# Kernel optimization log

Hardware: AMD Instinct MI355X
Metric: run time of the kernel (lower is better)

## Reference

```python
import jax, jax.numpy as jnp
from jax import lax
import numpy as np

N_NODES = 5000
N_EDGES = 80000
N_FEAT = 128
N_TPLT = 16
TPLT_NODES = 10
N_FW = 3         # Frank-Wolfe (conditional-gradient) outer iterations
SINK_ITERS = 10  # log-domain Sinkhorn inner iterations


def setup_inputs() -> dict:
    key = jax.random.key(0)
    k1, k2, k3, k4, k5 = jax.random.split(key, 5)
    x = jax.random.normal(k1, (N_NODES, N_FEAT), jnp.float32)
    src = jax.random.randint(k2, (N_EDGES,), 0, N_NODES, jnp.int32)
    dst = jax.random.randint(k3, (N_EDGES,), 0, N_NODES, jnp.int32)
    edge_index = jnp.stack([src, dst], axis=0)
    A0 = jax.random.uniform(k4, (N_TPLT, TPLT_NODES, TPLT_NODES), jnp.float32)
    tplt_adjacencies = 0.5 * (A0 + jnp.transpose(A0, (0, 2, 1)))  # symmetrized, as in template_initialisation
    tplt_features = jax.random.normal(k5, (N_TPLT, TPLT_NODES, N_FEAT), jnp.float32)
    q0 = jnp.zeros((N_TPLT, TPLT_NODES), jnp.float32)   # softmax(q0) -> uniform template node weights
    alpha0 = jnp.zeros((1,), jnp.float32)               # sigmoid(alpha0) -> alpha = 0.5
    return {"x": x, "edge_index": edge_index, "tplt_adjacencies": tplt_adjacencies,
            "tplt_features": tplt_features, "q0": q0, "alpha0": alpha0}


def _sinkhorn_log(G, logp, logq, reg):
    """Log-domain Sinkhorn solving min <G,T> + reg*KL(T | p q^T); returns T [N, m]."""
    def step(carry, _):
        f, g = carry
        f = reg * (logp - jax.scipy.special.logsumexp((g[None, :] - G) / reg, axis=1))
        g = reg * (logq - jax.scipy.special.logsumexp((f[:, None] - G) / reg, axis=0))
        return (f, g), None
    (f, g), _ = lax.scan(step, (jnp.zeros_like(logp), jnp.zeros_like(logq)), None, length=SINK_ITERS)
    return jnp.exp((f[:, None] + g[None, :] - G) / reg)


def _fgw_dist(A, x, p, C2, F2, q, alpha):
    """Fused Gromov-Wasserstein distance (square loss) between graph (A, x, p)
    and one template (C2, F2, q), solved by conditional gradient with Sinkhorn
    inner OT solves and exact quadratic line search."""
    # pairwise squared-euclidean feature cost M [N, m]
    M = jnp.sum(x * x, 1)[:, None] + jnp.sum(F2 * F2, 1)[None, :] - 2.0 * (x @ F2.T)
    # square-loss Gromov decomposition: L(C1,C2) (x) T = constC - 2 * C1 T C2
    constC = ((A * A) @ p)[:, None] + ((C2 * C2) @ q)[None, :]
    logp, logq = jnp.log(p), jnp.log(q)
    T0 = p[:, None] * q[None, :]

    def fw_step(T, _):
        ATC = A @ (T @ C2)                        # [N, m]
        tens = constC - 2.0 * ATC
        G = (1.0 - alpha) * M + 2.0 * alpha * tens  # linearized gradient
        reg = 0.05 * jnp.mean(jnp.abs(G)) + 1e-9
        Tn = _sinkhorn_log(G, logp, logq, reg)
        dT = Tn - T
        AdTC = A @ (dT @ C2)
        # cost(T + g*dT) = a g^2 + b g + c  (square-loss FGW)
        a = -2.0 * alpha * jnp.sum(AdTC * dT)
        b = (1.0 - alpha) * jnp.sum(M * dT) + alpha * (jnp.sum(constC * dT) - 4.0 * jnp.sum(ATC * dT))
        gamma = jnp.where(a > 0.0, jnp.clip(-b / (2.0 * a + 1e-16), 0.0, 1.0),
                          jnp.where(a + b < 0.0, 1.0, 0.0))
        return T + gamma * dT, None

    T, _ = lax.scan(fw_step, T0, None, length=N_FW)
    ATC = A @ (T @ C2)
    return (1.0 - alpha) * jnp.sum(M * T) + alpha * (jnp.sum(constC * T) - 2.0 * jnp.sum(ATC * T))


def reference(x, edge_index, tplt_adjacencies, tplt_features, q0, alpha0):
    N = x.shape[0]
    # dense adjacency from COO edge list (to_dense_adj equivalent)
    A = jnp.zeros((N, N), x.dtype).at[edge_index[0], edge_index[1]].set(1.0)
    p = jnp.full((N,), 1.0 / N, x.dtype)       # uniform graph node weights
    alpha = jax.nn.sigmoid(alpha0[0])          # trained FGW trade-off (multi_alpha=False)
    q = jax.nn.softmax(q0, axis=1)             # trained template node weights
    dists = jax.vmap(lambda C2, F2, qk: _fgw_dist(A, x, p, C2, F2, qk, alpha))(
        tplt_adjacencies, tplt_features, q)
    return dists  # [n_tplt] FGW-distance embedding of the graph
```

## Files before the change

### kernel.cpp

```cpp
#include <hip/hip_runtime.h>
#include <stdint.h>

typedef float    f32x4 __attribute__((ext_vector_type(4)));
typedef uint32_t u32x4 __attribute__((ext_vector_type(4)));

#define NN 5000
#define NE 80000
#define NF 128
#define NT 16
#define TN 10
#define NFW 3
#define NSK 10
#define PW (1.0f/5000.0f)
#define RB 128
#define GRX 40
#define TPB 1024
#define NSL 5

#define OFF_DEG  0u
#define OFF_RP   20224u
#define OFF_CUR  40448u
#define OFF_COL  60672u
#define OFF_SCG  380672u
#define OFF_M    384000u
#define OFF_T    4224000u
#define OFF_ATM  8064000u
#define OFF_ATT  9344000u
#define OFF_DTM  9664000u
#define OFF_DTT  10944000u
#define OFF_Y2M  11264000u
#define OFF_Y2T  12544000u
#define OFF_ADM  12864000u
#define OFF_ADT  14144000u

#define L_YM   0
#define L_YT   80000
#define L_RED  100000
#define L_WLS  101024
#define L_UNI  101088
#define SMEM_BYTES 101280

__device__ __forceinline__ uint32_t bfb(float x) {
  uint32_t u = __float_as_uint(x);
  return (u + 0x7fffu + ((u >> 16) & 1u)) >> 16;
}
__device__ __forceinline__ uint32_t pk(float a, float b) { return bfb(a) | (bfb(b) << 16); }
__device__ __forceinline__ float ubl(uint32_t u) { return __uint_as_float(u << 16); }
__device__ __forceinline__ float ubh(uint32_t u) { return __uint_as_float(u & 0xffff0000u); }
__device__ __forceinline__ float sigm(float z) { return 1.f / (1.f + __expf(-z)); }

__device__ __forceinline__ void ld12(const float* p, float* v) {
  f32x4 a = *(const f32x4*)p, b = *(const f32x4*)(p + 4), c = *(const f32x4*)(p + 8);
  v[0]=a[0]; v[1]=a[1]; v[2]=a[2]; v[3]=a[3]; v[4]=b[0]; v[5]=b[1]; v[6]=b[2]; v[7]=b[3];
  v[8]=c[0]; v[9]=c[1];
}
__device__ __forceinline__ void st12(float* p, const float* v) {
  *(f32x4*)p       = (f32x4){v[0], v[1], v[2], v[3]};
  *(f32x4*)(p + 4) = (f32x4){v[4], v[5], v[6], v[7]};
  *(f32x4*)(p + 8) = (f32x4){v[8], v[9], 0.f, 0.f};
}
__device__ __forceinline__ void ldbf(const u32x4* __restrict__ M4, const uint32_t* __restrict__ M1,
                                     size_t i, float* v) {
  u32x4 A = M4[i]; uint32_t B = M1[i];
  v[0]=ubl(A[0]); v[1]=ubh(A[0]); v[2]=ubl(A[1]); v[3]=ubh(A[1]);
  v[4]=ubl(A[2]); v[5]=ubh(A[2]); v[6]=ubl(A[3]); v[7]=ubh(A[3]);
  v[8]=ubl(B);    v[9]=ubh(B);
}
__device__ __forceinline__ void stbf(u32x4* __restrict__ M4, uint32_t* __restrict__ M1,
                                     size_t i, const float* v) {
  M4[i] = (u32x4){pk(v[0], v[1]), pk(v[2], v[3]), pk(v[4], v[5]), pk(v[6], v[7])};
  M1[i] = pk(v[8], v[9]);
}
__device__ __forceinline__ float bred16(float v, float* red) {
  #pragma unroll
  for (int o = 32; o; o >>= 1) v += __shfl_xor(v, o, 64);
  __syncthreads();
  if ((threadIdx.x & 63) == 0) red[threadIdx.x >> 6] = v;
  __syncthreads();
  float r = 0.f;
  #pragma unroll
  for (int w = 0; w < 16; ++w) r += red[w];
  return r;
}

__global__ void k_init(int* __restrict__ deg) {
  int i = blockIdx.x * 256 + threadIdx.x;
  if (i < NN) deg[i] = 0;
}
__global__ void k_deg(const int* __restrict__ ei, int* __restrict__ deg) {
  int e = blockIdx.x * 256 + threadIdx.x;
  if (e < NE) atomicAdd(&deg[ei[e]], 1);
}
__global__ void k_scan(const int* __restrict__ deg, int* __restrict__ rowptr, int* __restrict__ cur) {
  __shared__ int scr[1024];
  int tid = threadIdx.x;
  int loc[5], s = 0;
  #pragma unroll
  for (int r = 0; r < 5; ++r) {
    int idx = tid * 5 + r;
    int d = (idx < NN) ? deg[idx] : 0;
    loc[r] = s; s += d;
  }
  scr[tid] = s; __syncthreads();
  for (int off = 1; off < 1024; off <<= 1) {
    int v = scr[tid];
    int u = (tid >= off) ? scr[tid - off] : 0;
    __syncthreads();
    scr[tid] = v + u;
    __syncthreads();
  }
  int base = (tid > 0) ? scr[tid - 1] : 0;
  #pragma unroll
  for (int r = 0; r < 5; ++r) {
    int idx = tid * 5 + r;
    if (idx < NN) { int v = base + loc[r]; rowptr[idx] = v; cur[idx] = v; }
  }
  if (tid == 1023) rowptr[NN] = scr[1023];
}
__global__ void k_fill(const int* __restrict__ ei, int* __restrict__ cur, int* __restrict__ col) {
  int e = blockIdx.x * 256 + threadIdx.x;
  if (e < NE) {
    int s = ei[e];
    int pos = atomicAdd(&cur[s], 1);
    col[pos] = ei[NE + e];
  }
}
__global__ void kM(const float* __restrict__ x, const float* __restrict__ F2,
                   float* __restrict__ Mb) {
  __shared__ float ffs[TN];
  const int k = blockIdx.y, tid = threadIdx.x;
  const int i = blockIdx.x * RB + tid;
  const float* Fk = F2 + (size_t)k * TN * NF;
  if (tid < TN) {
    float s = 0.f;
    for (int d = 0; d < NF; ++d) { float f = Fk[tid * NF + d]; s += f * f; }
    ffs[tid] = s;
  }
  __syncthreads();
  if (i >= NN) return;
  const f32x4* xr = (const f32x4*)(x + (size_t)i * NF);
  float acc[TN];
  #pragma unroll
  for (int j = 0; j < TN; ++j) acc[j] = 0.f;
  float xsq = 0.f;
  for (int dc = 0; dc < NF / 4; ++dc) {
    f32x4 xv = xr[dc];
    xsq += xv[0]*xv[0] + xv[1]*xv[1] + xv[2]*xv[2] + xv[3]*xv[3];
    #pragma unroll
    for (int j = 0; j < TN; ++j) {
      const float* Fj = Fk + j * NF + dc * 4;
      acc[j] += xv[0]*Fj[0] + xv[1]*Fj[1] + xv[2]*Fj[2] + xv[3]*Fj[3];
    }
  }
  float v[TN];
  #pragma unroll
  for (int j = 0; j < TN; ++j) v[j] = xsq + ffs[j] - 2.f * acc[j];
  st12(Mb + ((size_t)k * NN + i) * 12, v);
}

__device__ __forceinline__ void uni_setup(const float* __restrict__ q0,
                                          const float* __restrict__ C2k, int k,
                                          float* qvs, float* c2qs, float* qC2s) {
  const int tid = threadIdx.x;
  if (tid < TN) {
    float mx = -1e30f, e[TN], s = 0.f;
    #pragma unroll
    for (int j = 0; j < TN; ++j) mx = fmaxf(mx, q0[k * TN + j]);
    #pragma unroll
    for (int j = 0; j < TN; ++j) { e[j] = __expf(q0[k * TN + j] - mx); s += e[j]; }
    float inv = 1.f / s;
    qvs[tid] = e[tid] * inv;
    float c2 = 0.f, qc = 0.f;
    #pragma unroll
    for (int l = 0; l < TN; ++l) {
      float c = C2k[tid * TN + l];
      c2 += c * c * e[l] * inv;
      qc += e[l] * inv * C2k[l * TN + tid];
    }
    c2qs[tid] = c2; qC2s[tid] = qc;
  }
  __syncthreads();
}

__global__ __launch_bounds__(TPB) void kFW(
    const int* __restrict__ rowptr, const int* __restrict__ col,
    const float* __restrict__ Mb, float* __restrict__ Tb,
    u32x4* __restrict__ AtM, uint32_t* __restrict__ AtT,
    u32x4* __restrict__ DtM, uint32_t* __restrict__ DtT,
    u32x4* __restrict__ Y2M, uint32_t* __restrict__ Y2T,
    u32x4* __restrict__ AdM, uint32_t* __restrict__ AdT_,
    const float* __restrict__ q0, const float* __restrict__ C2g,
    const float* __restrict__ a0p, float* __restrict__ scg, int t) {
  extern __shared__ char smem[];
  u32x4* LYM = (u32x4*)(smem + L_YM);
  uint32_t* LYT = (uint32_t*)(smem + L_YT);
  float* red = (float*)(smem + L_RED);
  float* wls = (float*)(smem + L_WLS);
  float* qvs = (float*)(smem + L_UNI);
  float* c2qs = qvs + 16; float* qC2s = qvs + 32;

  const int k = blockIdx.x, tid = threadIdx.x;
  const float* C2k = C2g + k * 100;
  uni_setup(q0, C2k, k, qvs, c2qs, qC2s);
  const float alpha = sigm(a0p[0]), oma = 1.f - alpha;
  const size_t kb = (size_t)k * NN;

  float gamma = 0.f;
  if (t > 0) {
    for (int i = tid; i < NN; i += TPB) { LYM[i] = Y2M[kb + i]; LYT[i] = Y2T[kb + i]; }
    __syncthreads();
    float bA = 0.f, aA = 0.f;
    for (int s = 0; s < NSL; ++s) {
      int r = s * TPB + tid;
      if (r < NN) {
        int e0 = rowptr[r], e1 = rowptr[r + 1];
        float adt[TN];
        #pragma unroll
        for (int j = 0; j < TN; ++j) adt[j] = 0.f;
        for (int e = e0; e < e1; ++e) {
          int c = col[e];
          u32x4 A = LYM[c]; uint32_t B = LYT[c];
          adt[0] += ubl(A[0]); adt[1] += ubh(A[0]); adt[2] += ubl(A[1]); adt[3] += ubh(A[1]);
          adt[4] += ubl(A[2]); adt[5] += ubh(A[2]); adt[6] += ubl(A[3]); adt[7] += ubh(A[3]);
          adt[8] += ubl(B);    adt[9] += ubh(B);
        }
        float av[TN], dv[TN];
        ldbf(AtM, AtT, kb + r, av); ldbf(DtM, DtT, kb + r, dv);
        #pragma unroll
        for (int j = 0; j < TN; ++j) { bA += av[j] * dv[j]; aA += adt[j] * dv[j]; }
        stbf(AdM, AdT_, kb + r, adt);
      }
    }
    bA = bred16(bA, red); aA = bred16(aA, red);
    const float bM = scg[k * 2 + 0], bC = scg[k * 2 + 1];
    float a_ = -2.f * alpha * aA;
    float b_ = oma * bM + alpha * (bC - 4.f * bA);
    gamma = (a_ > 0.f) ? fminf(fmaxf(-b_ / (2.f * a_ + 1e-16f), 0.f), 1.f)
                       : ((a_ + b_ < 0.f) ? 1.f : 0.f);
    for (int s = 0; s < NSL; ++s) {
      int r = s * TPB + tid;
      if (r < NN) {
        float tv[TN], dv[TN], av[TN], adt[TN];
        ld12(Tb + (kb + r) * 12, tv);
        ldbf(DtM, DtT, kb + r, dv);
        ldbf(AtM, AtT, kb + r, av);
        ldbf(AdM, AdT_, kb + r, adt);
        #pragma unroll
        for (int j = 0; j < TN; ++j) { tv[j] += gamma * dv[j]; av[j] += gamma * adt[j]; }
        st12(Tb + (kb + r) * 12, tv);
        stbf(AtM, AtT, kb + r, av);
      }
    }
  } else {
    for (int s = 0; s < NSL; ++s) {
      int r = s * TPB + tid;
      if (r < NN) {
        float dg = (float)(rowptr[r + 1] - rowptr[r]) * PW;
        float tv[TN], av[TN];
        #pragma unroll
        for (int j = 0; j < TN; ++j) { tv[j] = PW * qvs[j]; av[j] = dg * qC2s[j]; }
        st12(Tb + (kb + r) * 12, tv);
        stbf(AtM, AtT, kb + r, av);
      }
    }
  }

  float sabs = 0.f;
  for (int s = 0; s < NSL; ++s) {
    int r = s * TPB + tid;
    if (r < NN) {
      float mv[TN], av[TN];
      ld12(Mb + (kb + r) * 12, mv); ldbf(AtM, AtT, kb + r, av);
      float cc = (float)(rowptr[r + 1] - rowptr[r]) * PW;
      #pragma unroll
      for (int j = 0; j < TN; ++j)
        sabs += fabsf(oma * mv[j] + 2.f * alpha * (cc + c2qs[j] - 2.f * av[j]));
    }
  }
  sabs = bred16(sabs, red);
  const float invreg = 1.f / (0.05f * sabs * (1.f / (float)(NN * TN)) + 1e-9f);

  for (int s = 0; s < NSL; ++s) {
    int r = s * TPB + tid;
    if (r < NN) {
      float mv[TN], av[TN], G[TN];
      ld12(Mb + (kb + r) * 12, mv); ldbf(AtM, AtT, kb + r, av);
      float cc = (float)(rowptr[r + 1] - rowptr[r]) * PW;
      #pragma unroll
      for (int j = 0; j < TN; ++j)
        G[j] = oma * mv[j] + 2.f * alpha * (cc + c2qs[j] - 2.f * av[j]);
      float mn = G[0];
      #pragma unroll
      for (int j = 1; j < TN; ++j) mn = fminf(mn, G[j]);
      #pragma unroll
      for (int j = 0; j < TN; ++j) G[j] = __expf(-(G[j] - mn) * invreg);
      stbf(LYM, LYT, (size_t)r, G);
    }
  }
  __syncthreads();

  float wl[TN], wp[TN];
  #pragma unroll
  for (int j = 0; j < TN; ++j) { wl[j] = 1.f; wp[j] = 1.f; }
  for (int it = 0; it < NSK; ++it) {
    float csl[TN];
    #pragma unroll
    for (int j = 0; j < TN; ++j) csl[j] = 0.f;
    for (int s = 0; s < NSL; ++s) {
      int r = s * TPB + tid;
      if (r < NN) {
        float E[TN];
        ldbf(LYM, LYT, (size_t)r, E);
        float dot = 0.f;
        #pragma unroll
        for (int j = 0; j < TN; ++j) dot += E[j] * wl[j];
        float u = PW * __builtin_amdgcn_rcpf(fmaxf(dot, 1e-35f));
        #pragma unroll
        for (int j = 0; j < TN; ++j) csl[j] += E[j] * u;
      }
    }
    #pragma unroll
    for (int j = 0; j < TN; ++j) {
      float vv = csl[j];
      #pragma unroll
      for (int o = 32; o; o >>= 1) vv += __shfl_xor(vv, o, 64);
      if ((tid & 63) == j) red[(tid >> 6) * 16 + j] = vv;
    }
    __syncthreads();
    if (tid < TN) {
      float ssum = 0.f;
      #pragma unroll
      for (int w = 0; w < 16; ++w) ssum += red[w * 16 + tid];
      wls[tid] = qvs[tid] * __builtin_amdgcn_rcpf(fmaxf(ssum, 1e-35f));
    }
    __syncthreads();
    #pragma unroll
    for (int j = 0; j < TN; ++j) { wp[j] = wl[j]; wl[j] = wls[j]; }
  }

  float bM = 0.f, bC = 0.f;
  for (int s = 0; s < NSL; ++s) {
    int r = s * TPB + tid;
    if (r < NN) {
      float E[TN];
      ldbf(LYM, LYT, (size_t)r, E);
      float dot = 0.f;
      #pragma unroll
      for (int j = 0; j < TN; ++j) dot += E[j] * wp[j];
      float u = PW * __builtin_amdgcn_rcpf(fmaxf(dot, 1e-35f));
      float tv[TN], mv[TN], dT[TN];
      ld12(Tb + (kb + r) * 12, tv);
      ld12(Mb + (kb + r) * 12, mv);
      float cc = (float)(rowptr[r + 1] - rowptr[r]) * PW;
      #pragma unroll
      for (int j = 0; j < TN; ++j) {
        float tn = u * E[j] * wl[j];
        dT[j] = tn - tv[j];
        bM += mv[j] * dT[j];
        bC += (cc + c2qs[j]) * dT[j];
      }
      stbf(DtM, DtT, kb + r, dT);
      float y[TN];
      #pragma unroll
      for (int j = 0; j < TN; ++j) {
        float ss = 0.f;
        #pragma unroll
        for (int l = 0; l < TN; ++l) ss += dT[l] * C2k[l * TN + j];
        y[j] = ss;
      }
      stbf(Y2M, Y2T, kb + r, y);
    }
  }
  bM = bred16(bM, red); bC = bred16(bC, red);
  if (tid == 0) { scg[k * 2 + 0] = bM; scg[k * 2 + 1] = bC; }
}

__global__ __launch_bounds__(TPB) void kFin(
    const int* __restrict__ rowptr, const int* __restrict__ col,
    const float* __restrict__ Mb, const float* __restrict__ Tb,
    const u32x4* __restrict__ AtM, const uint32_t* __restrict__ AtT,
    const u32x4* __restrict__ DtM, const uint32_t* __restrict__ DtT,
    const u32x4* __restrict__ Y2M, const uint32_t* __restrict__ Y2T,
    u32x4* __restrict__ AdM, uint32_t* __restrict__ AdT_,
    const float* __restrict__ q0, const float* __restrict__ C2g,
    const float* __restrict__ a0p, const float* __restrict__ scg,
    float* __restrict__ out) {
  extern __shared__ char smem[];
  u32x4* LYM = (u32x4*)(smem + L_YM);
  uint32_t* LYT = (uint32_t*)(smem + L_YT);
  float* red = (float*)(smem + L_RED);
  float* qvs = (float*)(smem + L_UNI);
  float* c2qs = qvs + 16; float* qC2s = qvs + 32;

  const int k = blockIdx.x, tid = threadIdx.x;
  const float* C2k = C2g + k * 100;
  uni_setup(q0, C2k, k, qvs, c2qs, qC2s);
  const float alpha = sigm(a0p[0]), oma = 1.f - alpha;
  const size_t kb = (size_t)k * NN;

  for (int i = tid; i < NN; i += TPB) { LYM[i] = Y2M[kb + i]; LYT[i] = Y2T[kb + i]; }
  __syncthreads();
  float bA = 0.f, aA = 0.f;
  for (int s = 0; s < NSL; ++s) {
    int r = s * TPB + tid;
    if (r < NN) {
      int e0 = rowptr[r], e1 = rowptr[r + 1];
      float adt[TN];
      #pragma unroll
      for (int j = 0; j < TN; ++j) adt[j] = 0.f;
      for (int e = e0; e < e1; ++e) {
        int c = col[e];
        u32x4 A = LYM[c]; uint32_t B = LYT[c];
        adt[0] += ubl(A[0]); adt[1] += ubh(A[0]); adt[2] += ubl(A[1]); adt[3] += ubh(A[1]);
        adt[4] += ubl(A[2]); adt[5] += ubh(A[2]); adt[6] += ubl(A[3]); adt[7] += ubh(A[3]);
        adt[8] += ubl(B);    adt[9] += ubh(B);
      }
      float av[TN], dv[TN];
      ldbf(AtM, AtT, kb + r, av); ldbf(DtM, DtT, kb + r, dv);
      #pragma unroll
      for (int j = 0; j < TN; ++j) { bA += av[j] * dv[j]; aA += adt[j] * dv[j]; }
      stbf(AdM, AdT_, kb + r, adt);
    }
  }
  bA = bred16(bA, red); aA = bred16(aA, red);
  const float bM = scg[k * 2 + 0], bC = scg[k * 2 + 1];
  float a_ = -2.f * alpha * aA;
  float b_ = oma * bM + alpha * (bC - 4.f * bA);
  float gamma = (a_ > 0.f) ? fminf(fmaxf(-b_ / (2.f * a_ + 1e-16f), 0.f), 1.f)
                           : ((a_ + b_ < 0.f) ? 1.f : 0.f);
  float d1 = 0.f, d2 = 0.f, d3 = 0.f;
  for (int s = 0; s < NSL; ++s) {
    int r = s * TPB + tid;
    if (r < NN) {
      float tv[TN], dv[TN], av[TN], adt[TN], mv[TN];
      ld12(Tb + (kb + r) * 12, tv);
      ldbf(DtM, DtT, kb + r, dv);
      ldbf(AtM, AtT, kb + r, av);
      ldbf(AdM, AdT_, kb + r, adt);
      ld12(Mb + (kb + r) * 12, mv);
      float cc = (float)(rowptr[r + 1] - rowptr[r]) * PW;
      #pragma unroll
      for (int j = 0; j < TN; ++j) {
        float Tf = tv[j] + gamma * dv[j];
        float Af = av[j] + gamma * adt[j];
        d1 += mv[j] * Tf;
        d2 += (cc + c2qs[j]) * Tf;
        d3 += Af * Tf;
      }
    }
  }
  d1 = bred16(d1, red); d2 = bred16(d2, red); d3 = bred16(d3, red);
  if (tid == 0) out[k] = oma * d1 + alpha * (d2 - 2.f * d3);
}

extern "C" void kernel_launch(void* const* d_in, const int* in_sizes, int n_in,
                              void* d_out, int out_size, void* d_ws, size_t ws_size,
                              hipStream_t stream) {
  const float* x  = (const float*)d_in[0];
  const int*   ei = (const int*)d_in[1];
  const float* C2 = (const float*)d_in[2];
  const float* F2 = (const float*)d_in[3];
  const float* q0 = (const float*)d_in[4];
  const float* a0p = (const float*)d_in[5];
  float* out = (float*)d_out;

  char* ws = (char*)d_ws;
  int* deg    = (int*)(ws + OFF_DEG);
  int* rowptr = (int*)(ws + OFF_RP);
  int* cur    = (int*)(ws + OFF_CUR);
  int* col    = (int*)(ws + OFF_COL);
  float* scg  = (float*)(ws + OFF_SCG);
  float* Mb   = (float*)(ws + OFF_M);
  float* Tb   = (float*)(ws + OFF_T);
  u32x4* AtM  = (u32x4*)(ws + OFF_ATM);
  uint32_t* AtT = (uint32_t*)(ws + OFF_ATT);
  u32x4* DtM  = (u32x4*)(ws + OFF_DTM);
  uint32_t* DtT = (uint32_t*)(ws + OFF_DTT);
  u32x4* Y2M  = (u32x4*)(ws + OFF_Y2M);
  uint32_t* Y2T = (uint32_t*)(ws + OFF_Y2T);
  u32x4* AdM  = (u32x4*)(ws + OFF_ADM);
  uint32_t* AdT_ = (uint32_t*)(ws + OFF_ADT);

  hipFuncSetAttribute((const void*)kFW, hipFuncAttributeMaxDynamicSharedMemorySize, SMEM_BYTES);
  hipFuncSetAttribute((const void*)kFin, hipFuncAttributeMaxDynamicSharedMemorySize, SMEM_BYTES);

  k_init<<<(NN + 255) / 256, 256, 0, stream>>>(deg);
  k_deg<<<(NE + 255) / 256, 256, 0, stream>>>(ei, deg);
  k_scan<<<1, 1024, 0, stream>>>(deg, rowptr, cur);
  k_fill<<<(NE + 255) / 256, 256, 0, stream>>>(ei, cur, col);
  kM<<<dim3(GRX, NT), RB, 0, stream>>>(x, F2, Mb);

  for (int t = 0; t < NFW; ++t)
    kFW<<<NT, TPB, SMEM_BYTES, stream>>>(rowptr, col, Mb, Tb, AtM, AtT, DtM, DtT,
                                         Y2M, Y2T, AdM, AdT_, q0, C2, a0p, scg, t);
  kFin<<<NT, TPB, SMEM_BYTES, stream>>>(rowptr, col, Mb, Tb, AtM, AtT, DtM, DtT,
                                        Y2M, Y2T, AdM, AdT_, q0, C2, a0p, scg, out);
}
```

Baseline: 439.0 us.

## Split per-template FW kernel into multi-block stages with atomic cross-block reductions

Replaces the single 16-block kernel, which ran one 1024-thread block per template, with separate stage kernels. The gather A·ΔT (kA), the gradient/T update (kB) and the final objective (kFin) each run on a 40x16 grid, and the Sinkhorn kernel kD uses 16 blocks per template that each write only their own slice of rows. Partial sums are combined through global atomics, and a last-block counter produces the final output. M and the gradient are stored in fp16 to cut memory traffic. This spreads the work across far more CUs, at the cost of extra launches, redundant Sinkhorn iterations in every block of a template, and lower precision for M and G.

```diff
diff --git a/kernel.cpp b/kernel.cpp
--- a/kernel.cpp
+++ b/kernel.cpp
@@ -1,4 +1,5 @@
 #include <hip/hip_runtime.h>
+#include <hip/hip_fp16.h>
 #include <stdint.h>
 
 typedef float    f32x4 __attribute__((ext_vector_type(4)));
@@ -14,31 +15,37 @@
 #define PW (1.0f/5000.0f)
 #define RB 128
 #define GRX 40
-#define TPB 1024
-#define NSL 5
+#define DTPB 512
+#define DSL 10
+#define NBD 16
+#define RPD 313
 
 #define OFF_DEG  0u
 #define OFF_RP   20224u
 #define OFF_CUR  40448u
 #define OFF_COL  60672u
-#define OFF_SCG  380672u
-#define OFF_M    384000u
-#define OFF_T    4224000u
-#define OFF_ATM  8064000u
-#define OFF_ATT  9344000u
-#define OFF_DTM  9664000u
-#define OFF_DTT  10944000u
-#define OFF_Y2M  11264000u
-#define OFF_Y2T  12544000u
-#define OFF_ADM  12864000u
-#define OFF_ADT  14144000u
-
-#define L_YM   0
-#define L_YT   80000
+#define OFF_SC   380672u
+#define SC_FLOATS 384
+#define OFF_MM   382272u
+#define OFF_MT   1662272u
+#define OFF_T    1982272u
+#define OFF_ATM  5822272u
+#define OFF_ATT  7102272u
+#define OFF_DTM  7422272u
+#define OFF_DTT  8702272u
+#define OFF_Y2M  9022272u
+#define OFF_Y2T  10302272u
+#define OFF_ADM  10622272u
+#define OFF_ADT  11902272u
+#define OFF_GM   12222272u
+#define OFF_GT   13502272u
+
+#define L_EM   0
+#define L_ET   80000
 #define L_RED  100000
-#define L_WLS  101024
-#define L_UNI  101088
-#define SMEM_BYTES 101280
+#define L_WLS  100512
+#define L_UNI  100576
+#define SMEM_D 100768
 
 __device__ __forceinline__ uint32_t bfb(float x) {
   uint32_t u = __float_as_uint(x);
@@ -47,6 +54,16 @@
 __device__ __forceinline__ uint32_t pk(float a, float b) { return bfb(a) | (bfb(b) << 16); }
 __device__ __forceinline__ float ubl(uint32_t u) { return __uint_as_float(u << 16); }
 __device__ __forceinline__ float ubh(uint32_t u) { return __uint_as_float(u & 0xffff0000u); }
+__device__ __forceinline__ uint32_t pkh(float a, float b) {
+  return (uint32_t)__half_as_ushort(__float2half(a)) |
+         ((uint32_t)__half_as_ushort(__float2half(b)) << 16);
+}
+__device__ __forceinline__ float ulh(uint32_t u) {
+  return __half2float(__ushort_as_half((unsigned short)(u & 0xffffu)));
+}
+__device__ __forceinline__ float uhh(uint32_t u) {
+  return __half2float(__ushort_as_half((unsigned short)(u >> 16)));
+}
 __device__ __forceinline__ float sigm(float z) { return 1.f / (1.f + __expf(-z)); }
 
 __device__ __forceinline__ void ld12(const float* p, float* v) {
@@ -71,7 +88,20 @@
   M4[i] = (u32x4){pk(v[0], v[1]), pk(v[2], v[3]), pk(v[4], v[5]), pk(v[6], v[7])};
   M1[i] = pk(v[8], v[9]);
 }
-__device__ __forceinline__ float bred16(float v, float* red) {
+__device__ __forceinline__ void ldhf(const u32x4* __restrict__ M4, const uint32_t* __restrict__ M1,
+                                     size_t i, float* v) {
+  u32x4 A = M4[i]; uint32_t B = M1[i];
+  v[0]=ulh(A[0]); v[1]=uhh(A[0]); v[2]=ulh(A[1]); v[3]=uhh(A[1]);
+  v[4]=ulh(A[2]); v[5]=uhh(A[2]); v[6]=ulh(A[3]); v[7]=uhh(A[3]);
+  v[8]=ulh(B);    v[9]=uhh(B);
+}
+__device__ __forceinline__ void sthf(u32x4* __restrict__ M4, uint32_t* __restrict__ M1,
+                                     size_t i, const float* v) {
+  M4[i] = (u32x4){pkh(v[0], v[1]), pkh(v[2], v[3]), pkh(v[4], v[5]), pkh(v[6], v[7])};
+  M1[i] = pkh(v[8], v[9]);
+}
+template<int W>
+__device__ __forceinline__ float bredw(float v, float* red) {
   #pragma unroll
   for (int o = 32; o; o >>= 1) v += __shfl_xor(v, o, 64);
   __syncthreads();
@@ -79,13 +109,44 @@
   __syncthreads();
   float r = 0.f;
   #pragma unroll
-  for (int w = 0; w < 16; ++w) r += red[w];
+  for (int w = 0; w < W; ++w) r += red[w];
   return r;
 }
-
-__global__ void k_init(int* __restrict__ deg) {
-  int i = blockIdx.x * 256 + threadIdx.x;
-  if (i < NN) deg[i] = 0;
+__device__ __forceinline__ void uni_setup(const float* __restrict__ q0,
+                                          const float* __restrict__ C2k, int k,
+                                          float* qvs, float* c2qs, float* qC2s) {
+  const int tid = threadIdx.x;
+  if (tid < TN) {
+    float mx = -1e30f, e[TN], s = 0.f;
+    #pragma unroll
+    for (int j = 0; j < TN; ++j) mx = fmaxf(mx, q0[k * TN + j]);
+    #pragma unroll
+    for (int j = 0; j < TN; ++j) { e[j] = __expf(q0[k * TN + j] - mx); s += e[j]; }
+    float inv = 1.f / s;
+    qvs[tid] = e[tid] * inv;
+    float c2 = 0.f, qc = 0.f;
+    #pragma unroll
+    for (int l = 0; l < TN; ++l) {
+      float c = C2k[tid * TN + l];
+      c2 += c * c * e[l] * inv;
+      qc += e[l] * inv * C2k[l * TN + tid];
+    }
+    c2qs[tid] = c2; qC2s[tid] = qc;
+  }
+  __syncthreads();
+}
+__device__ __forceinline__ float gamma_from(const float* dk, float alpha, float oma) {
+  float a_ = -2.f * alpha * dk[3];
+  float b_ = oma * dk[0] + alpha * (dk[1] - 4.f * dk[2]);
+  return (a_ > 0.f) ? fminf(fmaxf(-b_ / (2.f * a_ + 1e-16f), 0.f), 1.f)
+                    : ((a_ + b_ < 0.f) ? 1.f : 0.f);
+}
+
+__global__ void k_init(char* __restrict__ ws) {
+  int g = blockIdx.x * 256 + threadIdx.x;
+  if (g < NN) ((int*)(ws + OFF_DEG))[g] = 0;
+  int z = g - NN;
+  if (z >= 0 && z < SC_FLOATS) ((float*)(ws + OFF_SC))[z] = 0.f;
 }
 __global__ void k_deg(const int* __restrict__ ei, int* __restrict__ deg) {
   int e = blockIdx.x * 256 + threadIdx.x;
@@ -126,7 +187,7 @@
   }
 }
 __global__ void kM(const float* __restrict__ x, const float* __restrict__ F2,
-                   float* __restrict__ Mb) {
+                   u32x4* __restrict__ MM, uint32_t* __restrict__ MT) {
   __shared__ float ffs[TN];
   const int k = blockIdx.y, tid = threadIdx.x;
   const int i = blockIdx.x * RB + tid;
@@ -155,146 +216,96 @@
   float v[TN];
   #pragma unroll
   for (int j = 0; j < TN; ++j) v[j] = xsq + ffs[j] - 2.f * acc[j];
-  st12(Mb + ((size_t)k * NN + i) * 12, v);
-}
-
-__device__ __forceinline__ void uni_setup(const float* __restrict__ q0,
-                                          const float* __restrict__ C2k, int k,
-                                          float* qvs, float* c2qs, float* qC2s) {
-  const int tid = threadIdx.x;
-  if (tid < TN) {
-    float mx = -1e30f, e[TN], s = 0.f;
-    #pragma unroll
-    for (int j = 0; j < TN; ++j) mx = fmaxf(mx, q0[k * TN + j]);
-    #pragma unroll
-    for (int j = 0; j < TN; ++j) { e[j] = __expf(q0[k * TN + j] - mx); s += e[j]; }
-    float inv = 1.f / s;
-    qvs[tid] = e[tid] * inv;
-    float c2 = 0.f, qc = 0.f;
-    #pragma unroll
-    for (int l = 0; l < TN; ++l) {
-      float c = C2k[tid * TN + l];
-      c2 += c * c * e[l] * inv;
-      qc += e[l] * inv * C2k[l * TN + tid];
-    }
-    c2qs[tid] = c2; qC2s[tid] = qc;
-  }
-  __syncthreads();
-}
-
-__global__ __launch_bounds__(TPB) void kFW(
-    const int* __restrict__ rowptr, const int* __restrict__ col,
-    const float* __restrict__ Mb, float* __restrict__ Tb,
-    u32x4* __restrict__ AtM, uint32_t* __restrict__ AtT,
+  sthf(MM, MT, (size_t)k * NN + i, v);
+}
+
+__global__ __launch_bounds__(RB) void kB(
+    const int* __restrict__ rowptr,
+    const u32x4* __restrict__ MM, const uint32_t* __restrict__ MT,
+    float* __restrict__ Tb, u32x4* __restrict__ AtM, uint32_t* __restrict__ AtT,
+    const u32x4* __restrict__ DtM, const uint32_t* __restrict__ DtT,
+    const u32x4* __restrict__ AdM, const uint32_t* __restrict__ AdT_,
+    u32x4* __restrict__ GM, uint32_t* __restrict__ GT,
+    const float* __restrict__ q0, const float* __restrict__ C2g,
+    const float* __restrict__ a0p, float* __restrict__ sc, int t) {
+  __shared__ float qvs[16], c2qs[16], qC2s[16];
+  __shared__ float redl[2];
+  const int k = blockIdx.y, tid = threadIdx.x;
+  const int i = blockIdx.x * RB + tid;
+  uni_setup(q0, C2g + k * 100, k, qvs, c2qs, qC2s);
+  const float alpha = sigm(a0p[0]), oma = 1.f - alpha;
+  float sabs = 0.f;
+  if (i < NN) {
+    const size_t bi = (size_t)k * NN + i;
+    const int dg = rowptr[i + 1] - rowptr[i];
+    const float cc = (float)dg * PW;
+    float Trow[TN], Arow[TN];
+    if (t == 0) {
+      #pragma unroll
+      for (int j = 0; j < TN; ++j) { Trow[j] = PW * qvs[j]; Arow[j] = (float)dg * PW * qC2s[j]; }
+    } else {
+      const float* dk = sc + 64 + (size_t)(t - 1) * 64 + k * 4;
+      const float gamma = gamma_from(dk, alpha, oma);
+      float tv[TN], dv[TN], av[TN], adv[TN];
+      ld12(Tb + bi * 12, tv);
+      ldbf(DtM, DtT, bi, dv);
+      ldbf(AtM, AtT, bi, av);
+      ldbf(AdM, AdT_, bi, adv);
+      #pragma unroll
+      for (int j = 0; j < TN; ++j) { Trow[j] = tv[j] + gamma * dv[j]; Arow[j] = av[j] + gamma * adv[j]; }
+    }
+    st12(Tb + bi * 12, Trow);
+    stbf(AtM, AtT, bi, Arow);
+    float mv[TN], G[TN];
+    ldhf(MM, MT, bi, mv);
+    #pragma unroll
+    for (int j = 0; j < TN; ++j) {
+      G[j] = oma * mv[j] + 2.f * alpha * (cc + c2qs[j] - 2.f * Arow[j]);
+      sabs += fabsf(G[j]);
+    }
+    sthf(GM, GT, bi, G);
+  }
+  sabs = bredw<2>(sabs, redl);
+  if (tid == 0) atomicAdd(sc + t * NT + k, sabs);
+}
+
+__global__ __launch_bounds__(DTPB) void kD(
+    const int* __restrict__ rowptr, const float* __restrict__ Tb,
+    const u32x4* __restrict__ MM, const uint32_t* __restrict__ MT,
+    const u32x4* __restrict__ GM, const uint32_t* __restrict__ GT,
     u32x4* __restrict__ DtM, uint32_t* __restrict__ DtT,
     u32x4* __restrict__ Y2M, uint32_t* __restrict__ Y2T,
-    u32x4* __restrict__ AdM, uint32_t* __restrict__ AdT_,
     const float* __restrict__ q0, const float* __restrict__ C2g,
-    const float* __restrict__ a0p, float* __restrict__ scg, int t) {
+    const float* __restrict__ a0p, float* __restrict__ sc, int t) {
   extern __shared__ char smem[];
-  u32x4* LYM = (u32x4*)(smem + L_YM);
-  uint32_t* LYT = (uint32_t*)(smem + L_YT);
+  u32x4* EM = (u32x4*)(smem + L_EM);
+  uint32_t* ET = (uint32_t*)(smem + L_ET);
   float* red = (float*)(smem + L_RED);
   float* wls = (float*)(smem + L_WLS);
   float* qvs = (float*)(smem + L_UNI);
   float* c2qs = qvs + 16; float* qC2s = qvs + 32;
 
-  const int k = blockIdx.x, tid = threadIdx.x;
+  const int b = blockIdx.x, k = blockIdx.y, tid = threadIdx.x;
   const float* C2k = C2g + k * 100;
   uni_setup(q0, C2k, k, qvs, c2qs, qC2s);
-  const float alpha = sigm(a0p[0]), oma = 1.f - alpha;
   const size_t kb = (size_t)k * NN;
 
-  float gamma = 0.f;
-  if (t > 0) {
-    for (int i = tid; i < NN; i += TPB) { LYM[i] = Y2M[kb + i]; LYT[i] = Y2T[kb + i]; }
-    __syncthreads();
-    float bA = 0.f, aA = 0.f;
-    for (int s = 0; s < NSL; ++s) {
-      int r = s * TPB + tid;
-      if (r < NN) {
-        int e0 = rowptr[r], e1 = rowptr[r + 1];
-        float adt[TN];
-        #pragma unroll
-        for (int j = 0; j < TN; ++j) adt[j] = 0.f;
-        for (int e = e0; e < e1; ++e) {
-          int c = col[e];
-          u32x4 A = LYM[c]; uint32_t B = LYT[c];
-          adt[0] += ubl(A[0]); adt[1] += ubh(A[0]); adt[2] += ubl(A[1]); adt[3] += ubh(A[1]);
-          adt[4] += ubl(A[2]); adt[5] += ubh(A[2]); adt[6] += ubl(A[3]); adt[7] += ubh(A[3]);
-          adt[8] += ubl(B);    adt[9] += ubh(B);
-        }
-        float av[TN], dv[TN];
-        ldbf(AtM, AtT, kb + r, av); ldbf(DtM, DtT, kb + r, dv);
-        #pragma unroll
-        for (int j = 0; j < TN; ++j) { bA += av[j] * dv[j]; aA += adt[j] * dv[j]; }
-        stbf(AdM, AdT_, kb + r, adt);
-      }
-    }
-    bA = bred16(bA, red); aA = bred16(aA, red);
-    const float bM = scg[k * 2 + 0], bC = scg[k * 2 + 1];
-    float a_ = -2.f * alpha * aA;
-    float b_ = oma * bM + alpha * (bC - 4.f * bA);
-    gamma = (a_ > 0.f) ? fminf(fmaxf(-b_ / (2.f * a_ + 1e-16f), 0.f), 1.f)
-                       : ((a_ + b_ < 0.f) ? 1.f : 0.f);
-    for (int s = 0; s < NSL; ++s) {
-      int r = s * TPB + tid;
-      if (r < NN) {
-        float tv[TN], dv[TN], av[TN], adt[TN];
-        ld12(Tb + (kb + r) * 12, tv);
-        ldbf(DtM, DtT, kb + r, dv);
-        ldbf(AtM, AtT, kb + r, av);
-        ldbf(AdM, AdT_, kb + r, adt);
-        #pragma unroll
-        for (int j = 0; j < TN; ++j) { tv[j] += gamma * dv[j]; av[j] += gamma * adt[j]; }
-        st12(Tb + (kb + r) * 12, tv);
-        stbf(AtM, AtT, kb + r, av);
-      }
-    }
-  } else {
-    for (int s = 0; s < NSL; ++s) {
-      int r = s * TPB + tid;
-      if (r < NN) {
-        float dg = (float)(rowptr[r + 1] - rowptr[r]) * PW;
-        float tv[TN], av[TN];
-        #pragma unroll
-        for (int j = 0; j < TN; ++j) { tv[j] = PW * qvs[j]; av[j] = dg * qC2s[j]; }
-        st12(Tb + (kb + r) * 12, tv);
-        stbf(AtM, AtT, kb + r, av);
-      }
-    }
-  }
-
-  float sabs = 0.f;
-  for (int s = 0; s < NSL; ++s) {
-    int r = s * TPB + tid;
+  for (int i = tid; i < NN; i += DTPB) { EM[i] = GM[kb + i]; ET[i] = GT[kb + i]; }
+  __syncthreads();
+  const float invreg = 1.f / (0.05f * sc[t * NT + k] * (1.f / (float)(NN * TN)) + 1e-9f);
+
+  #pragma unroll
+  for (int s = 0; s < DSL; ++s) {
+    int r = s * DTPB + tid;
     if (r < NN) {
-      float mv[TN], av[TN];
-      ld12(Mb + (kb + r) * 12, mv); ldbf(AtM, AtT, kb + r, av);
-      float cc = (float)(rowptr[r + 1] - rowptr[r]) * PW;
-      #pragma unroll
-      for (int j = 0; j < TN; ++j)
-        sabs += fabsf(oma * mv[j] + 2.f * alpha * (cc + c2qs[j] - 2.f * av[j]));
-    }
-  }
-  sabs = bred16(sabs, red);
-  const float invreg = 1.f / (0.05f * sabs * (1.f / (float)(NN * TN)) + 1e-9f);
-
-  for (int s = 0; s < NSL; ++s) {
-    int r = s * TPB + tid;
-    if (r < NN) {
-      float mv[TN], av[TN], G[TN];
-      ld12(Mb + (kb + r) * 12, mv); ldbf(AtM, AtT, kb + r, av);
-      float cc = (float)(rowptr[r + 1] - rowptr[r]) * PW;
-      #pragma unroll
-      for (int j = 0; j < TN; ++j)
-        G[j] = oma * mv[j] + 2.f * alpha * (cc + c2qs[j] - 2.f * av[j]);
-      float mn = G[0];
-      #pragma unroll
-      for (int j = 1; j < TN; ++j) mn = fminf(mn, G[j]);
-      #pragma unroll
-      for (int j = 0; j < TN; ++j) G[j] = __expf(-(G[j] - mn) * invreg);
-      stbf(LYM, LYT, (size_t)r, G);
+      float g[TN];
+      ldhf(EM, ET, (size_t)r, g);
+      float mn = g[0];
+      #pragma unroll
+      for (int j = 1; j < TN; ++j) mn = fminf(mn, g[j]);
+      #pragma unroll
+      for (int j = 0; j < TN; ++j) g[j] = __expf(-(g[j] - mn) * invreg);
+      sthf(EM, ET, (size_t)r, g);
     }
   }
   __syncthreads();
@@ -306,11 +317,12 @@
     float csl[TN];
     #pragma unroll
     for (int j = 0; j < TN; ++j) csl[j] = 0.f;
-    for (int s = 0; s < NSL; ++s) {
-      int r = s * TPB + tid;
+    #pragma unroll
+    for (int s = 0; s < DSL; ++s) {
+      int r = s * DTPB + tid;
       if (r < NN) {
         float E[TN];
-        ldbf(LYM, LYT, (size_t)r, E);
+        ldhf(EM, ET, (size_t)r, E);
         float dot = 0.f;
         #pragma unroll
         for (int j = 0; j < TN; ++j) dot += E[j] * wl[j];
@@ -330,7 +342,7 @@
     if (tid < TN) {
       float ssum = 0.f;
       #pragma unroll
-      for (int w = 0; w < 16; ++w) ssum += red[w * 16 + tid];
+      for (int w = 0; w < DTPB / 64; ++w) ssum += red[w * 16 + tid];
       wls[tid] = qvs[tid] * __builtin_amdgcn_rcpf(fmaxf(ssum, 1e-35f));
     }
     __syncthreads();
@@ -339,18 +351,18 @@
   }
 
   float bM = 0.f, bC = 0.f;
-  for (int s = 0; s < NSL; ++s) {
-    int r = s * TPB + tid;
+  if (tid < RPD) {
+    int r = b * RPD + tid;
     if (r < NN) {
       float E[TN];
-      ldbf(LYM, LYT, (size_t)r, E);
+      ldhf(EM, ET, (size_t)r, E);
       float dot = 0.f;
       #pragma unroll
       for (int j = 0; j < TN; ++j) dot += E[j] * wp[j];
       float u = PW * __builtin_amdgcn_rcpf(fmaxf(dot, 1e-35f));
       float tv[TN], mv[TN], dT[TN];
       ld12(Tb + (kb + r) * 12, tv);
-      ld12(Mb + (kb + r) * 12, mv);
+      ldhf(MM, MT, kb + r, mv);
       float cc = (float)(rowptr[r + 1] - rowptr[r]) * PW;
       #pragma unroll
       for (int j = 0; j < TN; ++j) {
@@ -371,86 +383,114 @@
       stbf(Y2M, Y2T, kb + r, y);
     }
   }
-  bM = bred16(bM, red); bC = bred16(bC, red);
-  if (tid == 0) { scg[k * 2 + 0] = bM; scg[k * 2 + 1] = bC; }
-}
-
-__global__ __launch_bounds__(TPB) void kFin(
+  bM = bredw<DTPB / 64>(bM, red);
+  bC = bredw<DTPB / 64>(bC, red);
+  if (tid == 0) {
+    float* dk = sc + 64 + (size_t)t * 64 + k * 4;
+    atomicAdd(dk + 0, bM);
+    atomicAdd(dk + 1, bC);
+  }
+}
+
+__global__ __launch_bounds__(RB) void kA(
     const int* __restrict__ rowptr, const int* __restrict__ col,
-    const float* __restrict__ Mb, const float* __restrict__ Tb,
+    const u32x4* __restrict__ Y2M, const uint32_t* __restrict__ Y2T,
     const u32x4* __restrict__ AtM, const uint32_t* __restrict__ AtT,
     const u32x4* __restrict__ DtM, const uint32_t* __restrict__ DtT,
-    const u32x4* __restrict__ Y2M, const uint32_t* __restrict__ Y2T,
     u32x4* __restrict__ AdM, uint32_t* __restrict__ AdT_,
+    float* __restrict__ sc, int tt) {
+  __shared__ float redl[2];
+  const int k = blockIdx.y, tid = threadIdx.x;
+  const int i = blockIdx.x * RB + tid;
+  float bA = 0.f, aA = 0.f;
+  if (i < NN) {
+    const size_t bi = (size_t)k * NN + i;
+    const u32x4* YM = Y2M + (size_t)k * NN;
+    const uint32_t* YT = Y2T + (size_t)k * NN;
+    int e0 = rowptr[i], e1 = rowptr[i + 1];
+    float adt[TN];
+    #pragma unroll
+    for (int j = 0; j < TN; ++j) adt[j] = 0.f;
+    for (int e = e0; e < e1; ++e) {
+      int c = col[e];
+      u32x4 A = YM[c]; uint32_t B = YT[c];
+      adt[0] += ubl(A[0]); adt[1] += ubh(A[0]); adt[2] += ubl(A[1]); adt[3] += ubh(A[1]);
+      adt[4] += ubl(A[2]); adt[5] += ubh(A[2]); adt[6] += ubl(A[3]); adt[7] += ubh(A[3]);
+      adt[8] += ubl(B);    adt[9] += ubh(B);
+    }
+    float av[TN], dv[TN];
+    ldbf(AtM, AtT, bi, av);
+    ldbf(DtM, DtT, bi, dv);
+    #pragma unroll
+    for (int j = 0; j < TN; ++j) { bA += av[j] * dv[j]; aA += adt[j] * dv[j]; }
+    stbf(AdM, AdT_, bi, adt);
+  }
+  bA = bredw<2>(bA, redl);
+  aA = bredw<2>(aA, redl);
+  if (tid == 0) {
+    float* dk = sc + 64 + (size_t)tt * 64 + k * 4;
+    atomicAdd(dk + 2, bA);
+    atomicAdd(dk + 3, aA);
+  }
+}
+
+__global__ __launch_bounds__(RB) void kFin(
+    const int* __restrict__ rowptr,
+    const u32x4* __restrict__ MM, const uint32_t* __restrict__ MT,
+    const float* __restrict__ Tb,
+    const u32x4* __restrict__ AtM, const uint32_t* __restrict__ AtT,
+    const u32x4* __restrict__ DtM, const uint32_t* __restrict__ DtT,
+    const u32x4* __restrict__ AdM, const uint32_t* __restrict__ AdT_,
     const float* __restrict__ q0, const float* __restrict__ C2g,
-    const float* __restrict__ a0p, const float* __restrict__ scg,
+    const float* __restrict__ a0p, float* __restrict__ sc,
     float* __restrict__ out) {
-  extern __shared__ char smem[];
-  u32x4* LYM = (u32x4*)(smem + L_YM);
-  uint32_t* LYT = (uint32_t*)(smem + L_YT);
-  float* red = (float*)(smem + L_RED);
-  float* qvs = (float*)(smem + L_UNI);
-  float* c2qs = qvs + 16; float* qC2s = qvs + 32;
-
-  const int k = blockIdx.x, tid = threadIdx.x;
-  const float* C2k = C2g + k * 100;
-  uni_setup(q0, C2k, k, qvs, c2qs, qC2s);
+  __shared__ float qvs[16], c2qs[16], qC2s[16];
+  __shared__ float redl[2];
+  const int k = blockIdx.y, tid = threadIdx.x;
+  const int i = blockIdx.x * RB + tid;
+  uni_setup(q0, C2g + k * 100, k, qvs, c2qs, qC2s);
   const float alpha = sigm(a0p[0]), oma = 1.f - alpha;
-  const size_t kb = (size_t)k * NN;
-
-  for (int i = tid; i < NN; i += TPB) { LYM[i] = Y2M[kb + i]; LYT[i] = Y2T[kb + i]; }
-  __syncthreads();
-  float bA = 0.f, aA = 0.f;
-  for (int s = 0; s < NSL; ++s) {
-    int r = s * TPB + tid;
-    if (r < NN) {
-      int e0 = rowptr[r], e1 = rowptr[r + 1];
-      float adt[TN];
-      #pragma unroll
-      for (int j = 0; j < TN; ++j) adt[j] = 0.f;
-      for (int e = e0; e < e1; ++e) {
-        int c = col[e];
-        u32x4 A = LYM[c]; uint32_t B = LYT[c];
-        adt[0] += ubl(A[0]); adt[1] += ubh(A[0]); adt[2] += ubl(A[1]); adt[3] += ubh(A[1]);
-        adt[4] += ubl(A[2]); adt[5] += ubh(A[2]); adt[6] += ubl(A[3]); adt[7] += ubh(A[3]);
-        adt[8] += ubl(B);    adt[9] += ubh(B);
-      }
-      float av[TN], dv[TN];
-      ldbf(AtM, AtT, kb + r, av); ldbf(DtM, DtT, kb + r, dv);
-      #pragma unroll
-      for (int j = 0; j < TN; ++j) { bA += av[j] * dv[j]; aA += adt[j] * dv[j]; }
-      stbf(AdM, AdT_, kb + r, adt);
-    }
-  }
-  bA = bred16(bA, red); aA = bred16(aA, red);
-  const float bM = scg[k * 2 + 0], bC = scg[k * 2 + 1];
-  float a_ = -2.f * alpha * aA;
-  float b_ = oma * bM + alpha * (bC - 4.f * bA);
-  float gamma = (a_ > 0.f) ? fminf(fmaxf(-b_ / (2.f * a_ + 1e-16f), 0.f), 1.f)
-                           : ((a_ + b_ < 0.f) ? 1.f : 0.f);
+  const float gamma = gamma_from(sc + 64 + (size_t)(NFW - 1) * 64 + k * 4, alpha, oma);
   float d1 = 0.f, d2 = 0.f, d3 = 0.f;
-  for (int s = 0; s < NSL; ++s) {
-    int r = s * TPB + tid;
-    if (r < NN) {
-      float tv[TN], dv[TN], av[TN], adt[TN], mv[TN];
-      ld12(Tb + (kb + r) * 12, tv);
-      ldbf(DtM, DtT, kb + r, dv);
-      ldbf(AtM, AtT, kb + r, av);
-      ldbf(AdM, AdT_, kb + r, adt);
-      ld12(Mb + (kb + r) * 12, mv);
-      float cc = (float)(rowptr[r + 1] - rowptr[r]) * PW;
-      #pragma unroll
-      for (int j = 0; j < TN; ++j) {
-        float Tf = tv[j] + gamma * dv[j];
-        float Af = av[j] + gamma * adt[j];
-        d1 += mv[j] * Tf;
-        d2 += (cc + c2qs[j]) * Tf;
-        d3 += Af * Tf;
-      }
-    }
-  }
-  d1 = bred16(d1, red); d2 = bred16(d2, red); d3 = bred16(d3, red);
-  if (tid == 0) out[k] = oma * d1 + alpha * (d2 - 2.f * d3);
+  if (i < NN) {
+    const size_t bi = (size_t)k * NN + i;
+    float tv[TN], dv[TN], av[TN], adv[TN], mv[TN];
+    ld12(Tb + bi * 12, tv);
+    ldbf(DtM, DtT, bi, dv);
+    ldbf(AtM, AtT, bi, av);
+    ldbf(AdM, AdT_, bi, adv);
+    ldhf(MM, MT, bi, mv);
+    float cc = (float)(rowptr[i + 1] - rowptr[i]) * PW;
+    #pragma unroll
+    for (int j = 0; j < TN; ++j) {
+      float Tf = tv[j] + gamma * dv[j];
+      float Af = av[j] + gamma * adv[j];
+      d1 += mv[j] * Tf;
+      d2 += (cc + c2qs[j]) * Tf;
+      d3 += Af * Tf;
+    }
+  }
+  d1 = bredw<2>(d1, redl);
+  d2 = bredw<2>(d2, redl);
+  d3 = bredw<2>(d3, redl);
+  float* fk = sc + 256 + k * 4;
+  if (tid == 0) {
+    atomicAdd(fk + 0, d1);
+    atomicAdd(fk + 1, d2);
+    atomicAdd(fk + 2, d3);
+  }
+  asm volatile("s_waitcnt vmcnt(0)" ::: "memory");
+  __syncthreads();
+  if (tid == 0) {
+    int* ctr = (int*)(sc + 320) + k;
+    int old = __hip_atomic_fetch_add(ctr, 1, __ATOMIC_RELAXED, __HIP_MEMORY_SCOPE_AGENT);
+    if (old == GRX - 1) {
+      float f0 = __hip_atomic_fetch_add(fk + 0, 0.f, __ATOMIC_RELAXED, __HIP_MEMORY_SCOPE_AGENT);
+      float f1 = __hip_atomic_fetch_add(fk + 1, 0.f, __ATOMIC_RELAXED, __HIP_MEMORY_SCOPE_AGENT);
+      float f2 = __hip_atomic_fetch_add(fk + 2, 0.f, __ATOMIC_RELAXED, __HIP_MEMORY_SCOPE_AGENT);
+      out[k] = oma * f0 + alpha * (f1 - 2.f * f2);
+    }
+  }
 }
 
 extern "C" void kernel_launch(void* const* d_in, const int* in_sizes, int n_in,
@@ -469,8 +509,9 @@
   int* rowptr = (int*)(ws + OFF_RP);
   int* cur    = (int*)(ws + OFF_CUR);
   int* col    = (int*)(ws + OFF_COL);
-  float* scg  = (float*)(ws + OFF_SCG);
-  float* Mb   = (float*)(ws + OFF_M);
+  float* sc   = (float*)(ws + OFF_SC);
+  u32x4* MM   = (u32x4*)(ws + OFF_MM);
+  uint32_t* MT = (uint32_t*)(ws + OFF_MT);
   float* Tb   = (float*)(ws + OFF_T);
   u32x4* AtM  = (u32x4*)(ws + OFF_ATM);
   uint32_t* AtT = (uint32_t*)(ws + OFF_ATT);
@@ -480,19 +521,31 @@
   uint32_t* Y2T = (uint32_t*)(ws + OFF_Y2T);
   u32x4* AdM  = (u32x4*)(ws + OFF_ADM);
   uint32_t* AdT_ = (uint32_t*)(ws + OFF_ADT);
-
-  hipFuncSetAttribute((const void*)kFW, hipFuncAttributeMaxDynamicSharedMemorySize, SMEM_BYTES);
-  hipFuncSetAttribute((const void*)kFin, hipFuncAttributeMaxDynamicSharedMemorySize, SMEM_BYTES);
-
-  k_init<<<(NN + 255) / 256, 256, 0, stream>>>(deg);
+  u32x4* GM   = (u32x4*)(ws + OFF_GM);
+  uint32_t* GT = (uint32_t*)(ws + OFF_GT);
+
+  hipFuncSetAttribute((const void*)kD, hipFuncAttributeMaxDynamicSharedMemorySize, SMEM_D);
+
+  const dim3 rg(GRX, NT), rb(RB);
+  const dim3 dg_(NBD, NT), db(DTPB);
+
+  k_init<<<(NN + SC_FLOATS + 255) / 256, 256, 0, stream>>>(ws);
   k_deg<<<(NE + 255) / 256, 256, 0, stream>>>(ei, deg);
   k_scan<<<1, 1024, 0, stream>>>(deg, rowptr, cur);
   k_fill<<<(NE + 255) / 256, 256, 0, stream>>>(ei, cur, col);
-  kM<<<dim3(GRX, NT), RB, 0, stream>>>(x, F2, Mb);
-
-  for (int t = 0; t < NFW; ++t)
-    kFW<<<NT, TPB, SMEM_BYTES, stream>>>(rowptr, col, Mb, Tb, AtM, AtT, DtM, DtT,
-                                         Y2M, Y2T, AdM, AdT_, q0, C2, a0p, scg, t);
-  kFin<<<NT, TPB, SMEM_BYTES, stream>>>(rowptr, col, Mb, Tb, AtM, AtT, DtM, DtT,
-                                        Y2M, Y2T, AdM, AdT_, q0, C2, a0p, scg, out);
-}
+  kM<<<rg, rb, 0, stream>>>(x, F2, MM, MT);
+
+  for (int t = 0; t < NFW; ++t) {
+    if (t > 0)
+      kA<<<rg, rb, 0, stream>>>(rowptr, col, Y2M, Y2T, AtM, AtT, DtM, DtT,
+                                AdM, AdT_, sc, t - 1);
+    kB<<<rg, rb, 0, stream>>>(rowptr, MM, MT, Tb, AtM, AtT, DtM, DtT, AdM, AdT_,
+                              GM, GT, q0, C2, a0p, sc, t);
+    kD<<<dg_, db, SMEM_D, stream>>>(rowptr, Tb, MM, MT, GM, GT, DtM, DtT,
+                                    Y2M, Y2T, q0, C2, a0p, sc, t);
+  }
+  kA<<<rg, rb, 0, stream>>>(rowptr, col, Y2M, Y2T, AtM, AtT, DtM, DtT,
+                            AdM, AdT_, sc, NFW - 1);
+  kFin<<<rg, rb, 0, stream>>>(rowptr, MM, MT, Tb, AtM, AtT, DtM, DtT, AdM, AdT_,
+                              q0, C2, a0p, sc, out);
+}
```

Result: faster. 370.8 us (-15.5%).
